# Kernel optimization log

Measured on AMD Instinct MI355X. Metric: run time of the kernel, lower is better.

## Reference

```python
import jax, jax.numpy as jnp
import numpy as np

WIN = 7  # window_size
NUM_HEADS = 8


def _relative_position_index(ws: int) -> np.ndarray:
    # Matches torch.meshgrid default ('ij') indexing used in the module.
    coords = np.stack(np.meshgrid(np.arange(ws), np.arange(ws), indexing='ij'))  # (2, ws, ws)
    flat = coords.reshape(2, -1)                                   # (2, ws*ws)
    rel = flat[:, :, None] - flat[:, None, :]                      # (2, N, N)
    rel = rel.transpose(1, 2, 0).copy()                            # (N, N, 2)
    rel[:, :, 0] += ws - 1
    rel[:, :, 1] += ws - 1
    rel[:, :, 0] *= 2 * ws - 1
    return rel.sum(-1)                                             # (N, N) int


def setup_inputs() -> dict:
    key = jax.random.key(0)
    ks = jax.random.split(key, 7)
    B_, N, C = 4096, WIN * WIN, 256
    nW = 64
    return {
        'x': jax.random.normal(ks[0], (B_, N, C), dtype=jnp.float32),
        'mask': jax.random.normal(ks[1], (nW, N, N), dtype=jnp.float32),
        'qkv_w': jax.random.normal(ks[2], (3 * C, C), dtype=jnp.float32) * 0.02,
        'qkv_b': jax.random.normal(ks[3], (3 * C,), dtype=jnp.float32) * 0.02,
        'proj_w': jax.random.normal(ks[4], (C, C), dtype=jnp.float32) * 0.02,
        'proj_b': jax.random.normal(ks[5], (C,), dtype=jnp.float32) * 0.02,
        'rpb_table': jax.random.normal(ks[6], ((2 * WIN - 1) ** 2, NUM_HEADS), dtype=jnp.float32) * 0.02,
    }


def reference(x, mask, qkv_w, qkv_b, proj_w, proj_b, rpb_table):
    B_, N, C = x.shape
    H = NUM_HEADS
    hd = C // H
    scale = hd ** -0.5
    rpi = jnp.asarray(_relative_position_index(WIN))  # (N, N) int, constant

    qkv = x @ qkv_w.T + qkv_b                          # (B_, N, 3C)
    qkv = qkv.reshape(B_, N, 3, H, hd).transpose(2, 0, 3, 1, 4)  # (3, B_, H, N, hd)
    q, k, v = qkv[0], qkv[1], qkv[2]

    attn = jnp.einsum('bhnd,bhmd->bhnm', q * scale, k)  # (B_, H, N, N)
    bias = rpb_table[rpi.reshape(-1)].reshape(N, N, H).transpose(2, 0, 1)  # (H, N, N)
    attn = attn + bias[None]

    nW = mask.shape[0]
    attn = attn.reshape(B_ // nW, nW, H, N, N) + mask[None, :, None]
    attn = attn.reshape(B_, H, N, N)
    attn = jax.nn.softmax(attn, axis=-1)

    out = jnp.einsum('bhnm,bhmd->bhnd', attn, v)       # (B_, H, N, hd)
    out = out.transpose(0, 2, 1, 3).reshape(B_, N, C)
    return out @ proj_w.T + proj_b
```

## Files before the change

kernel.cpp:

```cpp
#include <hip/hip_runtime.h>

#define SEG 51380224

typedef __attribute__((ext_vector_type(8))) __bf16 bf16x8;
typedef __attribute__((ext_vector_type(4))) __bf16 bf16x4;
typedef __attribute__((ext_vector_type(4))) float f32x4;

static __device__ __forceinline__ bf16x8 bzero8() {
    bf16x8 z;
#pragma unroll
    for (int u = 0; u < 8; ++u) z[u] = (__bf16)0.0f;
    return z;
}

static __device__ __forceinline__ void gl_lds16(const __bf16* g, __bf16* l) {
    __builtin_amdgcn_global_load_lds(
        (const __attribute__((address_space(1))) void*)g,
        (__attribute__((address_space(3))) void*)l, 16, 0, 0);
}

__global__ __launch_bounds__(256)
void cvt_bf16_k(const float* __restrict__ src, __bf16* __restrict__ dst, int n8)
{
    int i = blockIdx.x * 256 + threadIdx.x;
    const int stride = gridDim.x * 256;
    for (; i < n8; i += stride) {
        float4 a = *reinterpret_cast<const float4*>(src + (size_t)i * 8);
        float4 b = *reinterpret_cast<const float4*>(src + (size_t)i * 8 + 4);
        bf16x8 o;
        o[0] = (__bf16)a.x; o[1] = (__bf16)a.y; o[2] = (__bf16)a.z; o[3] = (__bf16)a.w;
        o[4] = (__bf16)b.x; o[5] = (__bf16)b.y; o[6] = (__bf16)b.z; o[7] = (__bf16)b.w;
        *reinterpret_cast<bf16x8*>(dst + (size_t)i * 8) = o;
    }
}

__global__ __launch_bounds__(256)
void expand_add_k(const float* __restrict__ mask, const float* __restrict__ rpb,
                  float* __restrict__ add)
{
    const int wh = blockIdx.x;
    const int w = wh >> 3, h = wh & 7;
    for (int e = threadIdx.x; e < 4096; e += 256) {
        int i = e >> 6, j = e & 63;
        float v = -1e30f;
        if (i < 49 && j < 49) {
            int ih = i / 7, iw = i - ih * 7;
            int jh = j / 7, jw = j - jh * 7;
            int bidx = (ih - jh + 6) * 13 + (iw - jw + 6);
            v = mask[(size_t)w * 2401 + i * 49 + j] + rpb[bidx * 8 + h];
        }
        add[(size_t)wh * 4096 + e] = v;
    }
}

__global__ __launch_bounds__(256)
void qkv_gemm_k(const __bf16* __restrict__ x, const __bf16* __restrict__ w,
                const float* __restrict__ bvec, __bf16* __restrict__ ws)
{
    __shared__ __bf16 As[2][128][64];
    __shared__ __bf16 Bs[2][128][64];
    const int tid  = threadIdx.x;
    const int nwg  = 1568 * 6;
    const int bid  = blockIdx.x;
    const int v    = (bid & 7) * (nwg >> 3) + (bid >> 3);
    const int mb   = v / 6, nb = v - mb * 6;
    const int m0   = mb * 128;
    const int n0   = nb * 128;
    const int wave = tid >> 6, lane = tid & 63;
    const int wm   = wave >> 1, wn = wave & 1;
    const int quad = lane >> 4, lm = lane & 15;

    const int srow = wave * 8 + (lane >> 3);
    const int scol = (((lane & 7) ^ (lane >> 3)) << 3);

    f32x4 acc[4][4] = {};

#pragma unroll
    for (int i = 0; i < 4; ++i) {
        int row = i * 32 + srow;
        gl_lds16(x + (size_t)(m0 + row) * 256 + 0 + scol,
                 &As[0][0][0] + i * 2048 + wave * 512);
        gl_lds16(w + (size_t)(n0 + row) * 256 + 0 + scol,
                 &Bs[0][0][0] + i * 2048 + wave * 512);
    }
    asm volatile("s_waitcnt vmcnt(0)" ::: "memory");
    __builtin_amdgcn_s_barrier();

#pragma unroll
    for (int t = 0; t < 4; ++t) {
        if (t < 3) {
            const int k0 = (t + 1) * 64;
            const int nb2 = (t + 1) & 1;
#pragma unroll
            for (int i = 0; i < 4; ++i) {
                int row = i * 32 + srow;
                gl_lds16(x + (size_t)(m0 + row) * 256 + k0 + scol,
                         &As[nb2][0][0] + i * 2048 + wave * 512);
                gl_lds16(w + (size_t)(n0 + row) * 256 + k0 + scol,
                         &Bs[nb2][0][0] + i * 2048 + wave * 512);
            }
        }
        const __bf16* Ab = &As[t & 1][0][0];
        const __bf16* Bb = &Bs[t & 1][0][0];
        __builtin_amdgcn_s_setprio(1);
#pragma unroll
        for (int kk = 0; kk < 64; kk += 32) {
            const int cl = (kk >> 3) + quad;
            bf16x8 af[4], bfr[4];
#pragma unroll
            for (int mt = 0; mt < 4; ++mt) {
                int row = wm * 64 + mt * 16 + lm;
                af[mt] = *reinterpret_cast<const bf16x8*>(Ab + row * 64 + ((cl ^ (lm & 7)) << 3));
            }
#pragma unroll
            for (int nt = 0; nt < 4; ++nt) {
                int row = wn * 64 + nt * 16 + lm;
                bfr[nt] = *reinterpret_cast<const bf16x8*>(Bb + row * 64 + ((cl ^ (lm & 7)) << 3));
            }
#pragma unroll
            for (int mt = 0; mt < 4; ++mt)
#pragma unroll
                for (int nt = 0; nt < 4; ++nt)
                    acc[mt][nt] = __builtin_amdgcn_mfma_f32_16x16x32_bf16(af[mt], bfr[nt], acc[mt][nt], 0, 0, 0);
        }
        __builtin_amdgcn_s_setprio(0);
        asm volatile("s_waitcnt vmcnt(0)" ::: "memory");
        __builtin_amdgcn_s_barrier();
    }

    const int   c3   = n0 >> 8;
    const float scl  = (c3 == 0) ? 0.17677669529663687f : 1.0f;
    __bf16*     segp = ws + (size_t)c3 * SEG;
    const int   n0c  = n0 & 255;
    char*       Cs   = (char*)&As[0][0][0];

#pragma unroll
    for (int nt = 0; nt < 4; ++nt) {
        float bj = bvec[n0 + wn * 64 + nt * 16 + lm];
#pragma unroll
        for (int mt = 0; mt < 4; ++mt)
#pragma unroll
            for (int r = 0; r < 4; ++r) {
                int row = wm * 64 + mt * 16 + quad * 4 + r;
                int byteoff = (row << 8) + ((wn * 64 + nt * 16 + lm) << 1);
                byteoff ^= (row & 0xC) << 2;
                *reinterpret_cast<__bf16*>(Cs + byteoff) =
                    (__bf16)((acc[mt][nt][r] + bj) * scl);
            }
    }
    __syncthreads();
#pragma unroll
    for (int it = 0; it < 8; ++it) {
        int row = it * 16 + (tid >> 4);
        int byteoff = (row << 8) + ((tid & 15) << 4);
        byteoff ^= (row & 0xC) << 2;
        bf16x8 c8 = *reinterpret_cast<const bf16x8*>(Cs + byteoff);
        *reinterpret_cast<bf16x8*>(segp + (size_t)(m0 + row) * 256 + n0c + ((tid & 15) << 3)) = c8;
    }
}

__global__ __launch_bounds__(64)
void attn_mfma_k(const __bf16* __restrict__ ws, const float* __restrict__ add,
                 __bf16* __restrict__ pre)
{
    __shared__ __bf16 Pl[64 * 72];
    __shared__ __bf16 Vt[32 * 72];
    const int lane = threadIdx.x;
    const int bh   = blockIdx.x;
    const int b    = bh >> 3, h = bh & 7;
    const int wh   = ((b & 63) << 3) | h;
    const int quad = lane >> 4, lm = lane & 15;
    const int koff = quad * 8;

    const __bf16* qp = ws + (size_t)(b * 49) * 256 + h * 32;
    const __bf16* kp = qp + SEG;
    const __bf16* vp = qp + (size_t)2 * SEG;

    {
        int d = lane >> 1, j0 = 48 + (lane & 1) * 8;
        *reinterpret_cast<bf16x8*>(&Vt[d * 72 + j0]) = bzero8();
    }
#pragma unroll
    for (int t = 0; t < 4; ++t) {
        int idx = lane + t * 64;
        if (idx < 196) {
            int j = idx >> 2, c8 = (idx & 3) * 8;
            bf16x8 vv = *reinterpret_cast<const bf16x8*>(vp + j * 256 + c8);
#pragma unroll
            for (int u = 0; u < 8; ++u) Vt[(c8 + u) * 72 + j] = vv[u];
        }
    }

    bf16x8 qf[4], kf[4];
#pragma unroll
    for (int t = 0; t < 4; ++t)
        qf[t] = *reinterpret_cast<const bf16x8*>(qp + (t * 16 + lm) * 256 + koff);
#pragma unroll
    for (int t = 0; t < 4; ++t) {
        int m = t * 16 + lm;
        kf[t] = (m < 49) ? *reinterpret_cast<const bf16x8*>(kp + m * 256 + koff)
                         : bzero8();
    }

    f32x4 s[4][4] = {};
#pragma unroll
    for (int mt = 0; mt < 4; ++mt)
#pragma unroll
        for (int nt = 0; nt < 4; ++nt)
            s[mt][nt] = __builtin_amdgcn_mfma_f32_16x16x32_bf16(kf[mt], qf[nt], s[mt][nt], 0, 0, 0);

    const float* ap = add + (size_t)wh * 4096;
#pragma unroll
    for (int nt = 0; nt < 4; ++nt) {
        int i = nt * 16 + lm;
#pragma unroll
        for (int mt = 0; mt < 4; ++mt) {
            f32x4 a4 = *reinterpret_cast<const f32x4*>(ap + i * 64 + mt * 16 + quad * 4);
            s[mt][nt] += a4;
        }
    }

#pragma unroll
    for (int nt = 0; nt < 4; ++nt) {
        float mx = -3.0e38f;
#pragma unroll
        for (int mt = 0; mt < 4; ++mt)
#pragma unroll
            for (int r = 0; r < 4; ++r) mx = fmaxf(mx, s[mt][nt][r]);
        mx = fmaxf(mx, __shfl_xor(mx, 16));
        mx = fmaxf(mx, __shfl_xor(mx, 32));
        float sum = 0.f;
#pragma unroll
        for (int mt = 0; mt < 4; ++mt)
#pragma unroll
            for (int r = 0; r < 4; ++r) {
                float e = __expf(s[mt][nt][r] - mx);
                s[mt][nt][r] = e; sum += e;
            }
        sum += __shfl_xor(sum, 16);
        sum += __shfl_xor(sum, 32);
        float rl = 1.0f / sum;
#pragma unroll
        for (int mt = 0; mt < 4; ++mt)
#pragma unroll
            for (int r = 0; r < 4; ++r) s[mt][nt][r] *= rl;
    }

#pragma unroll
    for (int nt = 0; nt < 4; ++nt) {
        int i = nt * 16 + lm;
#pragma unroll
        for (int mt = 0; mt < 4; ++mt) {
            bf16x4 p4;
#pragma unroll
            for (int r = 0; r < 4; ++r) p4[r] = (__bf16)s[mt][nt][r];
            *reinterpret_cast<bf16x4*>(&Pl[i * 72 + mt * 16 + quad * 4]) = p4;
        }
    }
    __syncthreads();

    f32x4 o[4][2] = {};
#pragma unroll
    for (int kt = 0; kt < 2; ++kt) {
        bf16x8 vf[2];
#pragma unroll
        for (int dt = 0; dt < 2; ++dt)
            vf[dt] = *reinterpret_cast<const bf16x8*>(&Vt[(dt * 16 + lm) * 72 + kt * 32 + koff]);
#pragma unroll
        for (int mt2 = 0; mt2 < 4; ++mt2) {
            bf16x8 pf = *reinterpret_cast<const bf16x8*>(&Pl[(mt2 * 16 + lm) * 72 + kt * 32 + koff]);
#pragma unroll
            for (int dt = 0; dt < 2; ++dt)
                o[mt2][dt] = __builtin_amdgcn_mfma_f32_16x16x32_bf16(pf, vf[dt], o[mt2][dt], 0, 0, 0);
        }
    }

    __syncthreads();
    __bf16* Ol = &Vt[0];
#pragma unroll
    for (int mt2 = 0; mt2 < 4; ++mt2)
#pragma unroll
        for (int dt = 0; dt < 2; ++dt)
#pragma unroll
            for (int r = 0; r < 4; ++r)
                Ol[(mt2 * 16 + quad * 4 + r) * 32 + dt * 16 + lm] = (__bf16)o[mt2][dt][r];
    __syncthreads();
#pragma unroll
    for (int it = 0; it < 4; ++it) {
        int i = it * 16 + (lane >> 2);
        if (i < 49) {
            bf16x8 v8 = *reinterpret_cast<const bf16x8*>(&Ol[i * 32 + (lane & 3) * 8]);
            *reinterpret_cast<bf16x8*>(pre + ((size_t)(b * 49 + i)) * 256 + h * 32 + (lane & 3) * 8) = v8;
        }
    }
}

__global__ __launch_bounds__(256)
void proj_gemm_k(const __bf16* __restrict__ pre, const __bf16* __restrict__ w,
                 const float* __restrict__ bvec, float* __restrict__ out)
{
    __shared__ __bf16 As[2][128][64];
    __shared__ __bf16 Bs[2][128][64];
    const int tid  = threadIdx.x;
    const int nwg  = 1568 * 2;
    const int bid  = blockIdx.x;
    const int v    = (bid & 7) * (nwg >> 3) + (bid >> 3);
    const int mb   = v >> 1, nb = v & 1;
    const int m0   = mb * 128;
    const int n0   = nb * 128;
    const int wave = tid >> 6, lane = tid & 63;
    const int wm   = wave >> 1, wn = wave & 1;
    const int quad = lane >> 4, lm = lane & 15;

    const int srow = wave * 8 + (lane >> 3);
    const int scol = (((lane & 7) ^ (lane >> 3)) << 3);

    f32x4 acc[4][4] = {};

#pragma unroll
    for (int i = 0; i < 4; ++i) {
        int row = i * 32 + srow;
        gl_lds16(pre + (size_t)(m0 + row) * 256 + 0 + scol,
                 &As[0][0][0] + i * 2048 + wave * 512);
        gl_lds16(w + (size_t)(n0 + row) * 256 + 0 + scol,
                 &Bs[0][0][0] + i * 2048 + wave * 512);
    }
    asm volatile("s_waitcnt vmcnt(0)" ::: "memory");
    __builtin_amdgcn_s_barrier();

#pragma unroll
    for (int t = 0; t < 4; ++t) {
        if (t < 3) {
            const int k0 = (t + 1) * 64;
            const int nb2 = (t + 1) & 1;
#pragma unroll
            for (int i = 0; i < 4; ++i) {
                int row = i * 32 + srow;
                gl_lds16(pre + (size_t)(m0 + row) * 256 + k0 + scol,
                         &As[nb2][0][0] + i * 2048 + wave * 512);
                gl_lds16(w + (size_t)(n0 + row) * 256 + k0 + scol,
                         &Bs[nb2][0][0] + i * 2048 + wave * 512);
            }
        }
        const __bf16* Ab = &As[t & 1][0][0];
        const __bf16* Bb = &Bs[t & 1][0][0];
        __builtin_amdgcn_s_setprio(1);
#pragma unroll
        for (int kk = 0; kk < 64; kk += 32) {
            const int cl = (kk >> 3) + quad;
            bf16x8 af[4], bfr[4];
#pragma unroll
            for (int mt = 0; mt < 4; ++mt) {
                int row = wm * 64 + mt * 16 + lm;
                af[mt] = *reinterpret_cast<const bf16x8*>(Ab + row * 64 + ((cl ^ (lm & 7)) << 3));
            }
#pragma unroll
            for (int nt = 0; nt < 4; ++nt) {
                int row = wn * 64 + nt * 16 + lm;
                bfr[nt] = *reinterpret_cast<const bf16x8*>(Bb + row * 64 + ((cl ^ (lm & 7)) << 3));
            }
#pragma unroll
            for (int mt = 0; mt < 4; ++mt)
#pragma unroll
                for (int nt = 0; nt < 4; ++nt)
                    acc[mt][nt] = __builtin_amdgcn_mfma_f32_16x16x32_bf16(af[mt], bfr[nt], acc[mt][nt], 0, 0, 0);
        }
        __builtin_amdgcn_s_setprio(0);
        asm volatile("s_waitcnt vmcnt(0)" ::: "memory");
        __builtin_amdgcn_s_barrier();
    }

#pragma unroll
    for (int nt = 0; nt < 4; ++nt) {
        int j = n0 + wn*64 + nt*16 + lm;
        float bj = bvec[j];
#pragma unroll
        for (int mt = 0; mt < 4; ++mt)
#pragma unroll
            for (int r = 0; r < 4; ++r) {
                int m = m0 + wm*64 + mt*16 + quad*4 + r;
                out[(size_t)m*256 + j] = acc[mt][nt][r] + bj;
            }
    }
}

extern "C" void kernel_launch(void* const* d_in, const int* in_sizes, int n_in,
                              void* d_out, int out_size, void* d_ws, size_t ws_size,
                              hipStream_t stream)
{
    const float* x      = (const float*)d_in[0];
    const float* mask   = (const float*)d_in[1];
    const float* qkv_w  = (const float*)d_in[2];
    const float* qkv_b  = (const float*)d_in[3];
    const float* proj_w = (const float*)d_in[4];
    const float* proj_b = (const float*)d_in[5];
    const float* rpb    = (const float*)d_in[6];

    __bf16* ws  = (__bf16*)d_ws;
    __bf16* pre = ws + (size_t)3 * SEG;
    float*  out = (float*)d_out;

    char*   ob      = (char*)d_out;
    float*  addbuf  = (float*)ob;
    __bf16* qkv_wb  = (__bf16*)(ob + (10u << 20));
    __bf16* xb      = (__bf16*)(ob + (16u << 20));
    __bf16* proj_wb = ws;

    cvt_bf16_k<<<dim3(2048), 256, 0, stream>>>(x, xb, 51380224 / 8);
    cvt_bf16_k<<<dim3(96),   256, 0, stream>>>(qkv_w, qkv_wb, 196608 / 8);
    expand_add_k<<<dim3(512), 256, 0, stream>>>(mask, rpb, addbuf);
    qkv_gemm_k<<<dim3(1568 * 6), 256, 0, stream>>>(xb, qkv_wb, qkv_b, ws);
    attn_mfma_k<<<dim3(32768), 64, 0, stream>>>(ws, addbuf, pre);
    cvt_bf16_k<<<dim3(32),   256, 0, stream>>>(proj_w, proj_wb, 65536 / 8);
    proj_gemm_k<<<dim3(1568 * 2), 256, 0, stream>>>(pre, proj_wb, proj_b, out);
}
```

Measured before the change: 781.6 us.

## Fuse fp32-to-bf16 conversion of x into the QKV GEMM A-tile load

```diff
diff --git a/kernel.cpp b/kernel.cpp
--- a/kernel.cpp
+++ b/kernel.cpp
@@ -54,7 +54,7 @@
 }
 
 __global__ __launch_bounds__(256)
-void qkv_gemm_k(const __bf16* __restrict__ x, const __bf16* __restrict__ w,
+void qkv_gemm_k(const float* __restrict__ x, const __bf16* __restrict__ w,
                 const float* __restrict__ bvec, __bf16* __restrict__ ws)
 {
     __shared__ __bf16 As[2][128][64];
@@ -73,32 +73,46 @@
     const int srow = wave * 8 + (lane >> 3);
     const int scol = (((lane & 7) ^ (lane >> 3)) << 3);
 
+    const int ar = tid >> 1;
+    const int ah = tid & 1;
+    const float* xrow = x + (size_t)(m0 + ar) * 256 + ah * 32;
+
     f32x4 acc[4][4] = {};
-
-#pragma unroll
-    for (int i = 0; i < 4; ++i) {
-        int row = i * 32 + srow;
-        gl_lds16(x + (size_t)(m0 + row) * 256 + 0 + scol,
-                 &As[0][0][0] + i * 2048 + wave * 512);
-        gl_lds16(w + (size_t)(n0 + row) * 256 + 0 + scol,
+    f32x4 a0[4], a1[4];
+
+#pragma unroll
+    for (int j = 0; j < 4; ++j) {
+        a0[j] = __builtin_nontemporal_load(reinterpret_cast<const f32x4*>(xrow + j * 8));
+        a1[j] = __builtin_nontemporal_load(reinterpret_cast<const f32x4*>(xrow + j * 8 + 4));
+    }
+#pragma unroll
+    for (int i = 0; i < 4; ++i)
+        gl_lds16(w + (size_t)(n0 + i * 32 + srow) * 256 + 0 + scol,
                  &Bs[0][0][0] + i * 2048 + wave * 512);
-    }
     asm volatile("s_waitcnt vmcnt(0)" ::: "memory");
-    __builtin_amdgcn_s_barrier();
+#pragma unroll
+    for (int j = 0; j < 4; ++j) {
+        bf16x8 o;
+        o[0] = (__bf16)a0[j][0]; o[1] = (__bf16)a0[j][1]; o[2] = (__bf16)a0[j][2]; o[3] = (__bf16)a0[j][3];
+        o[4] = (__bf16)a1[j][0]; o[5] = (__bf16)a1[j][1]; o[6] = (__bf16)a1[j][2]; o[7] = (__bf16)a1[j][3];
+        *reinterpret_cast<bf16x8*>(&As[0][ar][(((ah * 4 + j) ^ (ar & 7)) << 3)]) = o;
+    }
+    __syncthreads();
 
 #pragma unroll
     for (int t = 0; t < 4; ++t) {
+        const int nxt = (t + 1) & 1;
         if (t < 3) {
             const int k0 = (t + 1) * 64;
-            const int nb2 = (t + 1) & 1;
-#pragma unroll
-            for (int i = 0; i < 4; ++i) {
-                int row = i * 32 + srow;
-                gl_lds16(x + (size_t)(m0 + row) * 256 + k0 + scol,
-                         &As[nb2][0][0] + i * 2048 + wave * 512);
-                gl_lds16(w + (size_t)(n0 + row) * 256 + k0 + scol,
-                         &Bs[nb2][0][0] + i * 2048 + wave * 512);
-            }
+#pragma unroll
+            for (int j = 0; j < 4; ++j) {
+                a0[j] = __builtin_nontemporal_load(reinterpret_cast<const f32x4*>(xrow + k0 + j * 8));
+                a1[j] = __builtin_nontemporal_load(reinterpret_cast<const f32x4*>(xrow + k0 + j * 8 + 4));
+            }
+#pragma unroll
+            for (int i = 0; i < 4; ++i)
+                gl_lds16(w + (size_t)(n0 + i * 32 + srow) * 256 + k0 + scol,
+                         &Bs[nxt][0][0] + i * 2048 + wave * 512);
         }
         const __bf16* Ab = &As[t & 1][0][0];
         const __bf16* Bb = &Bs[t & 1][0][0];
@@ -125,7 +139,16 @@
         }
         __builtin_amdgcn_s_setprio(0);
         asm volatile("s_waitcnt vmcnt(0)" ::: "memory");
-        __builtin_amdgcn_s_barrier();
+        if (t < 3) {
+#pragma unroll
+            for (int j = 0; j < 4; ++j) {
+                bf16x8 o;
+                o[0] = (__bf16)a0[j][0]; o[1] = (__bf16)a0[j][1]; o[2] = (__bf16)a0[j][2]; o[3] = (__bf16)a0[j][3];
+                o[4] = (__bf16)a1[j][0]; o[5] = (__bf16)a1[j][1]; o[6] = (__bf16)a1[j][2]; o[7] = (__bf16)a1[j][3];
+                *reinterpret_cast<bf16x8*>(&As[nxt][ar][(((ah * 4 + j) ^ (ar & 7)) << 3)]) = o;
+            }
+        }
+        __syncthreads();
     }
 
     const int   c3   = n0 >> 8;
@@ -155,7 +178,8 @@
         int byteoff = (row << 8) + ((tid & 15) << 4);
         byteoff ^= (row & 0xC) << 2;
         bf16x8 c8 = *reinterpret_cast<const bf16x8*>(Cs + byteoff);
-        *reinterpret_cast<bf16x8*>(segp + (size_t)(m0 + row) * 256 + n0c + ((tid & 15) << 3)) = c8;
+        __builtin_nontemporal_store(c8,
+            reinterpret_cast<bf16x8*>(segp + (size_t)(m0 + row) * 256 + n0c + ((tid & 15) << 3)));
     }
 }
 
@@ -379,7 +403,7 @@
 #pragma unroll
             for (int r = 0; r < 4; ++r) {
                 int m = m0 + wm*64 + mt*16 + quad*4 + r;
-                out[(size_t)m*256 + j] = acc[mt][nt][r] + bj;
+                __builtin_nontemporal_store(acc[mt][nt][r] + bj, &out[(size_t)m*256 + j]);
             }
     }
 }
@@ -403,13 +427,11 @@
     char*   ob      = (char*)d_out;
     float*  addbuf  = (float*)ob;
     __bf16* qkv_wb  = (__bf16*)(ob + (10u << 20));
-    __bf16* xb      = (__bf16*)(ob + (16u << 20));
     __bf16* proj_wb = ws;
 
-    cvt_bf16_k<<<dim3(2048), 256, 0, stream>>>(x, xb, 51380224 / 8);
     cvt_bf16_k<<<dim3(96),   256, 0, stream>>>(qkv_w, qkv_wb, 196608 / 8);
     expand_add_k<<<dim3(512), 256, 0, stream>>>(mask, rpb, addbuf);
-    qkv_gemm_k<<<dim3(1568 * 6), 256, 0, stream>>>(xb, qkv_wb, qkv_b, ws);
+    qkv_gemm_k<<<dim3(1568 * 6), 256, 0, stream>>>(x, qkv_wb, qkv_b, ws);
     attn_mfma_k<<<dim3(32768), 64, 0, stream>>>(ws, addbuf, pre);
     cvt_bf16_k<<<dim3(32),   256, 0, stream>>>(proj_w, proj_wb, 65536 / 8);
     proj_gemm_k<<<dim3(1568 * 2), 256, 0, stream>>>(pre, proj_wb, proj_b, out);
```

New measurement: 967.8 us. 1.24x slower.
